# Optimization experiments

Measured on AMD Instinct MI355X. Metric: run time of the kernel, lower is better.

## Reference

```python
import jax, jax.numpy as jnp
import numpy as np
from jax import lax

INV_SQRT2 = np.float32(1.0 / np.sqrt(2.0))

def conv2d(x, w, b=None, stride=1, pad=0):
    y = lax.conv_general_dilated(x, w, (stride, stride), [(pad, pad), (pad, pad)],
                                 dimension_numbers=('NCHW', 'OIHW', 'NCHW'))
    return y if b is None else y + b[None, :, None, None]

def haar_dwt2_zero(x):
    # pytorch_wavelets DWTForward(J=1, wave='haar', mode='zero') for odd H,W:
    # pad one zero at the end of each spatial dim, then pairwise Haar analysis.
    x = jnp.pad(x, ((0, 0), (0, 0), (0, 1), (0, 1)))
    xe, xo = x[..., 0::2], x[..., 1::2]
    lo_w, hi_w = (xe + xo) * INV_SQRT2, (xe - xo) * INV_SQRT2
    def rows(t):
        te, to = t[:, :, 0::2, :], t[:, :, 1::2, :]
        return (te + to) * INV_SQRT2, (te - to) * INV_SQRT2
    ll, lh = rows(lo_w)
    hl, hh = rows(hi_w)
    return ll, lh, hl, hh  # cA, cH, cV, cD

def pixel_shuffle2(x):
    B, C, H, W = x.shape
    co = C // 4
    return x.reshape(B, co, 2, 2, H, W).transpose(0, 1, 4, 2, 5, 3).reshape(B, co, H * 2, W * 2)

def gaussian_kernel5(sigma=0.5):
    r = np.arange(5, dtype=np.float64) - 2.0
    k = np.exp(-(r ** 2) / (2.0 * sigma * sigma))
    return jnp.asarray((k / k.sum()).astype(np.float32))

_GK = gaussian_kernel5(0.5)

def gaussian_blur5(x4d):
    # cv2.GaussianBlur ksize=(5,5) sigma=0.5, default BORDER_REFLECT_101 -> 'reflect' pad
    p = jnp.pad(x4d, ((0, 0), (0, 0), (2, 2), (2, 2)), mode='reflect')
    p = conv2d(p, _GK.reshape(1, 1, 5, 1))
    return conv2d(p, _GK.reshape(1, 1, 1, 5))

def channel_attention(x, w1, w2):
    avg = jnp.mean(x, axis=(2, 3), keepdims=True)
    mx = jnp.max(x, axis=(2, 3), keepdims=True)
    mlp = lambda v: conv2d(jax.nn.relu(conv2d(v, w1)), w2)
    return jax.nn.sigmoid(mlp(avg) + mlp(mx)) * x

def _forward(x, w_x1, b_x1, w_x2, b_x2, w_x3, b_x3, w_hi, b_hi, w_lo, b_lo,
             ca1_w1, ca1_w2, ca2_w1, ca2_w2, w_cat, b_cat, w_c9a, b_c9a, w_c9b, b_c9b):
    f1 = jax.nn.relu(conv2d(x, w_x1, b_x1))            # (1,16,H,W)
    f2 = jax.nn.relu(conv2d(f1, w_x2, b_x2))           # (1,8,H,W)
    tmp12 = jax.nn.relu(conv2d(f2, w_x3, b_x3))        # (1,1,H,W)
    cA, cH, cV, cD = haar_dwt2_zero(tmp12)             # each (1,1,(H+1)/2,(W+1)/2)
    hf = pixel_shuffle2(jax.nn.relu(conv2d(jnp.concatenate([cH, cV, cD], 1), w_hi, b_hi, pad=1)))
    lf = pixel_shuffle2(jax.nn.relu(conv2d(cA, w_lo, b_lo, pad=1)))  # (1,1,H+5,W+5)
    # original detaches hf (cpu->numpy->cv2->cuda): gradients do not flow through it
    hf = gaussian_blur5(lax.stop_gradient(hf))
    hf = channel_attention(hf, ca1_w1, ca1_w2)
    lf = channel_attention(lf, ca2_w1, ca2_w2)
    alpha = 1.0
    cat = jax.nn.relu(conv2d(jnp.concatenate([alpha * hf, (1.0 - alpha) * lf], 1), w_cat, b_cat))
    f12 = tmp12 + cat                                   # (1,1,H,W)
    h = jax.nn.relu(conv2d(f12, w_c9a, b_c9a, pad=1))   # (1,32,H,W)
    return jax.nn.relu(conv2d(h, w_c9b, b_c9b, pad=1))  # (1,64,H,W)

def setup_inputs() -> dict:
    key = jax.random.key(0)
    ks = jax.random.split(key, 24)
    f32 = jnp.float32
    n = lambda k, s, sc=0.05: jax.random.normal(k, s, f32) * sc
    H = W = 511
    return {
        'x': jax.random.normal(ks[0], (1, 204, H, W), f32),
        'w_x1': n(ks[1], (16, 204, 1, 1)), 'b_x1': n(ks[2], (16,)),
        'w_x2': n(ks[3], (8, 16, 1, 1)),   'b_x2': n(ks[4], (8,)),
        'w_x3': n(ks[5], (1, 8, 1, 1)),    'b_x3': n(ks[6], (1,)),
        'w_hi': n(ks[7], (4, 3, 1, 1)),    'b_hi': n(ks[8], (4,)),
        'w_lo': n(ks[9], (4, 1, 1, 1)),    'b_lo': n(ks[10], (4,)),
        'ca1_w1': n(ks[11], (1, 1, 1, 1), 0.5), 'ca1_w2': n(ks[12], (1, 1, 1, 1), 0.5),
        'ca2_w1': n(ks[13], (1, 1, 1, 1), 0.5), 'ca2_w2': n(ks[14], (1, 1, 1, 1), 0.5),
        'w_cat': n(ks[15], (1, 2, 6, 6)),  'b_cat': n(ks[16], (1,)),
        'w_c9a': n(ks[17], (32, 1, 3, 3)), 'b_c9a': n(ks[18], (32,)),
        'w_c9b': n(ks[19], (64, 32, 3, 3)), 'b_c9b': n(ks[20], (64,)),
    }

def reference(x, w_x1, b_x1, w_x2, b_x2, w_x3, b_x3, w_hi, b_hi, w_lo, b_lo,
              ca1_w1, ca1_w2, ca2_w1, ca2_w2, w_cat, b_cat, w_c9a, b_c9a, w_c9b, b_c9b):
    return _forward(x, w_x1, b_x1, w_x2, b_x2, w_x3, b_x3, w_hi, b_hi, w_lo, b_lo,
                    ca1_w1, ca1_w2, ca2_w1, ca2_w2, w_cat, b_cat, w_c9a, b_c9a, w_c9b, b_c9b)
```

## Files before the change

kernel.cpp:

```cpp
#include <hip/hip_runtime.h>
#include <math.h>

#define NP 261121
#define WPX 520

typedef __attribute__((ext_vector_type(8))) short short8;
typedef __attribute__((ext_vector_type(4))) float f32x4;

static __device__ __forceinline__ unsigned short f2bf(float f) {
    unsigned int u = __builtin_bit_cast(unsigned int, f);
    u += 0x7FFFu + ((u >> 16) & 1u);
    return (unsigned short)(u >> 16);
}

__global__ __launch_bounds__(256) void k_prep(const float* __restrict__ w_c9a,
                                              const float* __restrict__ w_c9b,
                                              float* __restrict__ wTa,
                                              unsigned short* __restrict__ wb2)
{
    int t = blockIdx.x * 256 + threadIdx.x;
    if (t < 288) {
        int o = t & 31, k = t >> 5;
        wTa[t] = w_c9a[o * 9 + k];
    }
    if (t < 18432) {
        int o = t / 288, ck = t - o * 288;
        int c = ck / 9, k = ck - c * 9;
        wb2[k * 2048 + o * 32 + c] = f2bf(w_c9b[t]);
    }
}

__global__ __launch_bounds__(256) void k_zero(unsigned short* __restrict__ h2)
{
    int t = blockIdx.x * 256 + threadIdx.x;
    const int ROWN = WPX * 32;
    if (t < 2 * ROWN) {
        int r = t / ROWN;
        h2[(r ? 512 : 0) * ROWN + (t % ROWN)] = 0;
    }
    int u = t - 2 * ROWN;
    if (u >= 0 && u < 511 * 96) {
        int row = u / 96 + 1, cc = u - (u / 96) * 96;
        int col = (cc < 32) ? 0 : (cc < 64 ? 512 : 513);
        h2[(row * WPX + col) * 32 + (cc & 31)] = 0;
    }
}

__global__ __launch_bounds__(256) void k_conv123(const float* __restrict__ x,
                                                 const float* __restrict__ w1,
                                                 const float* __restrict__ b1,
                                                 const float* __restrict__ w2,
                                                 const float* __restrict__ b2,
                                                 const float* __restrict__ w3,
                                                 const float* __restrict__ b3,
                                                 float* __restrict__ tmp12)
{
    __shared__ float s_w1[204 * 16];
    __shared__ float s_misc[192];
    int t = threadIdx.x;
    for (int i = t; i < 204 * 16; i += 256)
        s_w1[i] = w1[(i & 15) * 204 + (i >> 4)];
    if (t < 128) s_misc[t] = w2[t];
    else if (t < 136) s_misc[t] = w3[t - 128];
    else if (t < 152) s_misc[t] = b1[t - 136];
    else if (t < 160) s_misc[t] = b2[t - 152];
    else if (t == 160) s_misc[160] = b3[0];
    __syncthreads();

    int p = blockIdx.x * 256 + t;
    if (p >= NP) return;

    float acc[16];
#pragma unroll
    for (int o = 0; o < 16; ++o) acc[o] = 0.f;

    const float* xp = x + p;
#pragma unroll 4
    for (int c = 0; c < 204; ++c) {
        float xv = xp[(size_t)c * NP];
        const float4* wv = reinterpret_cast<const float4*>(s_w1 + c * 16);
        float wl[16];
        *reinterpret_cast<float4*>(&wl[0])  = wv[0];
        *reinterpret_cast<float4*>(&wl[4])  = wv[1];
        *reinterpret_cast<float4*>(&wl[8])  = wv[2];
        *reinterpret_cast<float4*>(&wl[12]) = wv[3];
#pragma unroll
        for (int o = 0; o < 16; ++o) acc[o] = fmaf(xv, wl[o], acc[o]);
    }

    float f1[16];
#pragma unroll
    for (int o = 0; o < 16; ++o) f1[o] = fmaxf(acc[o] + s_misc[136 + o], 0.f);

    float tmp = s_misc[160];
#pragma unroll
    for (int j = 0; j < 8; ++j) {
        float s = s_misc[152 + j];
#pragma unroll
        for (int o = 0; o < 16; ++o) s = fmaf(f1[o], s_misc[j * 16 + o], s);
        tmp = fmaf(fmaxf(s, 0.f), s_misc[128 + j], tmp);
    }
    tmp12[p] = fmaxf(tmp, 0.f);
}

__global__ __launch_bounds__(256) void k_dwt_hi(const float* __restrict__ tmp12,
                                                const float* __restrict__ w_hi,
                                                const float* __restrict__ b_hi,
                                                float* __restrict__ hf)
{
    const float INV = 0.70710678118654752440f;
    int idx = blockIdx.x * 256 + threadIdx.x;
    if (idx >= 258 * 258) return;
    int h = idx / 258, w = idx - h * 258;

    float wh[12], bh[4];
#pragma unroll
    for (int i = 0; i < 12; ++i) wh[i] = w_hi[i];
#pragma unroll
    for (int o = 0; o < 4; ++o) bh[o] = b_hi[o];

    float v[4];
    if (h == 0 || h == 257 || w == 0 || w == 257) {
#pragma unroll
        for (int o = 0; o < 4; ++o) v[o] = fmaxf(bh[o], 0.f);
    } else {
        int hh = h - 1, ww = w - 1;
        int r0 = 2 * hh, r1 = 2 * hh + 1, c0 = 2 * ww, c1 = 2 * ww + 1;
        float a = tmp12[r0 * 511 + c0];
        float b = (c1 < 511) ? tmp12[r0 * 511 + c1] : 0.f;
        float c = (r1 < 511) ? tmp12[r1 * 511 + c0] : 0.f;
        float d = (r1 < 511 && c1 < 511) ? tmp12[r1 * 511 + c1] : 0.f;
        float lo0 = (a + b) * INV, hi0 = (a - b) * INV;
        float lo1 = (c + d) * INV, hi1 = (c - d) * INV;
        float cH = (lo0 - lo1) * INV;
        float cV = (hi0 + hi1) * INV;
        float cD = (hi0 - hi1) * INV;
#pragma unroll
        for (int o = 0; o < 4; ++o)
            v[o] = fmaxf(wh[o * 3 + 0] * cH + wh[o * 3 + 1] * cV + wh[o * 3 + 2] * cD + bh[o], 0.f);
    }
    int orow = (2 * h) * 516 + 2 * w;
    hf[orow]       = v[0];
    hf[orow + 1]   = v[1];
    hf[orow + 516] = v[2];
    hf[orow + 517] = v[3];
}

__global__ __launch_bounds__(256) void k_blur(const float* __restrict__ hf,
                                              float* __restrict__ hfb,
                                              float g0, float g1, float g2)
{
    int idx = blockIdx.x * 256 + threadIdx.x;
    if (idx >= 516 * 516) return;
    int y = idx / 516, x = idx - y * 516;
    float g[5] = {g0, g1, g2, g1, g0};
    int ry[5], rx[5];
#pragma unroll
    for (int i = 0; i < 5; ++i) {
        int yy = y + i - 2; yy = yy < 0 ? -yy : (yy > 515 ? 1030 - yy : yy);
        int xx = x + i - 2; xx = xx < 0 ? -xx : (xx > 515 ? 1030 - xx : xx);
        ry[i] = yy * 516; rx[i] = xx;
    }
    float s = 0.f;
#pragma unroll
    for (int i = 0; i < 5; ++i) {
        float rs = 0.f;
#pragma unroll
        for (int j = 0; j < 5; ++j) rs = fmaf(g[j], hf[ry[i] + rx[j]], rs);
        s = fmaf(g[i], rs, s);
    }
    hfb[idx] = s;
}

__global__ __launch_bounds__(256) void k_red1(const float* __restrict__ hfb,
                                              float* __restrict__ psum,
                                              float* __restrict__ pmax)
{
    __shared__ float ss[256], sm[256];
    int t = threadIdx.x;
    int gid = blockIdx.x * 256 + t;
    float s = 0.f, m = -3.4e38f;
    for (int i = gid; i < 516 * 516; i += 65536) { float v = hfb[i]; s += v; m = fmaxf(m, v); }
    ss[t] = s; sm[t] = m;
    __syncthreads();
    for (int off = 128; off > 0; off >>= 1) {
        if (t < off) { ss[t] += ss[t + off]; sm[t] = fmaxf(sm[t], sm[t + off]); }
        __syncthreads();
    }
    if (t == 0) { psum[blockIdx.x] = ss[0]; pmax[blockIdx.x] = sm[0]; }
}

__global__ __launch_bounds__(256) void k_red2(const float* __restrict__ psum,
                                              const float* __restrict__ pmax,
                                              const float* __restrict__ caw1,
                                              const float* __restrict__ caw2,
                                              float* __restrict__ scale)
{
    __shared__ float ss[256], sm[256];
    int t = threadIdx.x;
    ss[t] = psum[t]; sm[t] = pmax[t];
    __syncthreads();
    for (int off = 128; off > 0; off >>= 1) {
        if (t < off) { ss[t] += ss[t + off]; sm[t] = fmaxf(sm[t], sm[t + off]); }
        __syncthreads();
    }
    if (t == 0) {
        float avg = ss[0] / 266256.f;
        float mx = sm[0];
        float a = caw1[0], b = caw2[0];
        float z = b * fmaxf(a * avg, 0.f) + b * fmaxf(a * mx, 0.f);
        scale[0] = 1.f / (1.f + expf(-z));
    }
}

__global__ __launch_bounds__(256) void k_cat(const float* __restrict__ hfb,
                                             const float* __restrict__ tmp12,
                                             const float* __restrict__ w_cat,
                                             const float* __restrict__ b_cat,
                                             const float* __restrict__ scale,
                                             float* __restrict__ f12)
{
    int p = blockIdx.x * 256 + threadIdx.x;
    if (p >= NP) return;
    int y = p / 511, x = p - y * 511;
    float sc = scale[0];
    float s = 0.f;
#pragma unroll
    for (int ky = 0; ky < 6; ++ky) {
        const float* row = hfb + (y + ky) * 516 + x;
#pragma unroll
        for (int kx = 0; kx < 6; ++kx) s = fmaf(row[kx], w_cat[ky * 6 + kx], s);
    }
    f12[p] = tmp12[p] + fmaxf(sc * s + b_cat[0], 0.f);
}

__global__ __launch_bounds__(256) void k_c9a(const float* __restrict__ f12,
                                             const float* __restrict__ wTa,
                                             const float* __restrict__ bias,
                                             unsigned short* __restrict__ h2)
{
    int p = blockIdx.x * 256 + threadIdx.x;
    if (p >= NP) return;
    int y = p / 511, x = p - y * 511;
    float hv[9];
#pragma unroll
    for (int ky = 0; ky < 3; ++ky)
#pragma unroll
        for (int kx = 0; kx < 3; ++kx) {
            int yy = y + ky - 1, xx = x + kx - 1;
            hv[ky * 3 + kx] = (yy >= 0 && yy < 511 && xx >= 0 && xx < 511) ? f12[yy * 511 + xx] : 0.f;
        }
    float acc[32];
#pragma unroll
    for (int o = 0; o < 32; ++o) acc[o] = bias[o];
#pragma unroll
    for (int k = 0; k < 9; ++k) {
        float v = hv[k];
        const float* wp = wTa + k * 32;
#pragma unroll
        for (int o = 0; o < 32; ++o) acc[o] = fmaf(v, wp[o], acc[o]);
    }
    unsigned short o16[32];
#pragma unroll
    for (int o = 0; o < 32; ++o) o16[o] = f2bf(fmaxf(acc[o], 0.f));
    unsigned short* dst = h2 + ((size_t)(y + 1) * WPX + (x + 1)) * 32;
#pragma unroll
    for (int i = 0; i < 4; ++i)
        reinterpret_cast<short8*>(dst)[i] = reinterpret_cast<const short8*>(o16)[i];
}

__global__ __launch_bounds__(256, 2) void k_c9b(const unsigned short* __restrict__ h2,
                                                const unsigned short* __restrict__ wb2,
                                                const float* __restrict__ bias,
                                                float* __restrict__ out)
{
    int wave = threadIdx.x >> 6, lane = threadIdx.x & 63;
    int y  = blockIdx.x >> 1;
    int xh = blockIdx.x & 1;
    int xb = xh * 256 + wave * 64;
    int lpx = lane & 15, kg = lane >> 4;

    f32x4 acc[4][4];
#pragma unroll
    for (int m = 0; m < 4; ++m)
#pragma unroll
        for (int n = 0; n < 4; ++n) acc[m][n] = (f32x4){0.f, 0.f, 0.f, 0.f};

    const int base = (((y + 1) * WPX) + (xb + 1) + lpx) * 32 + kg * 8;

#pragma unroll
    for (int kt = 0; kt < 9; ++kt) {
        const int dy = kt / 3 - 1, dx = kt % 3 - 1;
        const int toff = (dy * WPX + dx) * 32;

        short8 a[4], b[4];
        const short8* wp = reinterpret_cast<const short8*>(wb2 + kt * 2048 + kg * 8);
#pragma unroll
        for (int m = 0; m < 4; ++m) a[m] = wp[(m * 16 + lpx) * 4];
#pragma unroll
        for (int n = 0; n < 4; ++n)
            b[n] = *reinterpret_cast<const short8*>(h2 + base + toff + n * 512);
#pragma unroll
        for (int m = 0; m < 4; ++m)
#pragma unroll
            for (int n = 0; n < 4; ++n)
                acc[m][n] = __builtin_amdgcn_mfma_f32_16x16x32_bf16(a[m], b[n], acc[m][n], 0, 0, 0);
    }

    const int ybase = y * 511;
#pragma unroll
    for (int m = 0; m < 4; ++m) {
#pragma unroll
        for (int r = 0; r < 4; ++r) {
            int o = m * 16 + kg * 4 + r;
            float bo = bias[o];
#pragma unroll
            for (int n = 0; n < 4; ++n) {
                int px = xb + n * 16 + lpx;
                if (px < 511)
                    out[(size_t)o * NP + ybase + px] = fmaxf(acc[m][n][r] + bo, 0.f);
            }
        }
    }
}

extern "C" void kernel_launch(void* const* d_in, const int* in_sizes, int n_in,
                              void* d_out, int out_size, void* d_ws, size_t ws_size,
                              hipStream_t stream)
{
    (void)in_sizes; (void)n_in; (void)out_size; (void)ws_size;

    const float* x     = (const float*)d_in[0];
    const float* w_x1  = (const float*)d_in[1];
    const float* b_x1  = (const float*)d_in[2];
    const float* w_x2  = (const float*)d_in[3];
    const float* b_x2  = (const float*)d_in[4];
    const float* w_x3  = (const float*)d_in[5];
    const float* b_x3  = (const float*)d_in[6];
    const float* w_hi  = (const float*)d_in[7];
    const float* b_hi  = (const float*)d_in[8];
    const float* ca1w1 = (const float*)d_in[11];
    const float* ca1w2 = (const float*)d_in[12];
    const float* w_cat = (const float*)d_in[15];
    const float* b_cat = (const float*)d_in[16];
    const float* w_c9a = (const float*)d_in[17];
    const float* b_c9a = (const float*)d_in[18];
    const float* w_c9b = (const float*)d_in[19];
    const float* b_c9b = (const float*)d_in[20];

    float* ws    = (float*)d_ws;
    float* tmp12 = ws + 0;
    float* hf    = ws + 261184;
    float* hfb   = ws + 527488;
    float* f12   = ws + 793792;
    float* psum  = ws + 1054976;
    float* pmax  = ws + 1055232;
    float* scale = ws + 1055488;
    float* wTa   = ws + 1055552;
    unsigned short* wb2 = (unsigned short*)(ws + 1055872);
    unsigned short* h2  = (unsigned short*)(ws + 1065088);

    float* out = (float*)d_out;

    double kk[5], ssum = 0.0;
    for (int i = 0; i < 5; ++i) { double r = i - 2.0; kk[i] = exp(-r * r / 0.5); ssum += kk[i]; }
    float g0 = (float)(kk[0] / ssum), g1 = (float)(kk[1] / ssum), g2 = (float)(kk[2] / ssum);

    k_prep<<<72, 256, 0, stream>>>(w_c9a, w_c9b, wTa, wb2);
    k_zero<<<322, 256, 0, stream>>>(h2);
    k_conv123<<<1021, 256, 0, stream>>>(x, w_x1, b_x1, w_x2, b_x2, w_x3, b_x3, tmp12);
    k_dwt_hi<<<261, 256, 0, stream>>>(tmp12, w_hi, b_hi, hf);
    k_blur<<<1041, 256, 0, stream>>>(hf, hfb, g0, g1, g2);
    k_red1<<<256, 256, 0, stream>>>(hfb, psum, pmax);
    k_red2<<<1, 256, 0, stream>>>(psum, pmax, ca1w1, ca1w2, scale);
    k_cat<<<1021, 256, 0, stream>>>(hfb, tmp12, w_cat, b_cat, scale, f12);
    k_c9a<<<1021, 256, 0, stream>>>(f12, wTa, b_c9a, h2);
    k_c9b<<<1022, 256, 0, stream>>>(h2, wb2, b_c9b, out);
}
```

Before: 123.4 us.

## Split h2 into channel planes, remap c9b blocks per XCD, merge zero kernel

The intermediate h2 buffer moves from pixel-interleaved 32 channels to four planes of 8 channels each, so each MFMA B-operand load in k_c9b reads a contiguous 16-byte chunk within a plane. Block IDs in k_c9b are remapped so consecutive rows land on the same XCD, which is meant to improve L2 reuse of the overlapping stencil rows. The halo-zeroing kernel is folded into k_prep, saving a launch. k_conv123 drops its LDS staging and instead reads a pretransposed weight array from global memory, relying on the scalar cache. This risks register pressure and slower weight reads in conv123.

```diff
diff --git a/kernel.cpp b/kernel.cpp
--- a/kernel.cpp
+++ b/kernel.cpp
@@ -1,8 +1,10 @@
 #include <hip/hip_runtime.h>
 #include <math.h>
 
-#define NP 261121
-#define WPX 520
+#define NP   261121
+#define WPX  520
+#define ROWN 4160
+#define PSTR 2138240
 
 typedef __attribute__((ext_vector_type(8))) short short8;
 typedef __attribute__((ext_vector_type(4))) float f32x4;
@@ -15,39 +17,40 @@
 
 __global__ __launch_bounds__(256) void k_prep(const float* __restrict__ w_c9a,
                                               const float* __restrict__ w_c9b,
+                                              const float* __restrict__ w_x1,
                                               float* __restrict__ wTa,
-                                              unsigned short* __restrict__ wb2)
+                                              unsigned short* __restrict__ wb2,
+                                              float* __restrict__ wT1,
+                                              unsigned short* __restrict__ h2)
 {
     int t = blockIdx.x * 256 + threadIdx.x;
-    if (t < 288) {
-        int o = t & 31, k = t >> 5;
-        wTa[t] = w_c9a[o * 9 + k];
-    }
+    if (t < 288)  wTa[t] = w_c9a[(t & 31) * 9 + (t >> 5)];
+    if (t < 3264) wT1[t] = w_x1[(t & 15) * 204 + (t >> 4)];
     if (t < 18432) {
         int o = t / 288, ck = t - o * 288;
         int c = ck / 9, k = ck - c * 9;
         wb2[k * 2048 + o * 32 + c] = f2bf(w_c9b[t]);
     }
-}
-
-__global__ __launch_bounds__(256) void k_zero(unsigned short* __restrict__ h2)
-{
-    int t = blockIdx.x * 256 + threadIdx.x;
-    const int ROWN = WPX * 32;
-    if (t < 2 * ROWN) {
-        int r = t / ROWN;
-        h2[(r ? 512 : 0) * ROWN + (t % ROWN)] = 0;
-    }
-    int u = t - 2 * ROWN;
-    if (u >= 0 && u < 511 * 96) {
-        int row = u / 96 + 1, cc = u - (u / 96) * 96;
-        int col = (cc < 32) ? 0 : (cc < 64 ? 512 : 513);
-        h2[(row * WPX + col) * 32 + (cc & 31)] = 0;
+    short8 z8 = {0, 0, 0, 0, 0, 0, 0, 0};
+    if (t < 4160) {
+        int pl = t / 1040;
+        int rr = t - pl * 1040;
+        int row = rr >= 520 ? 512 : 0;
+        int ch  = rr >= 520 ? rr - 520 : rr;
+        *reinterpret_cast<short8*>(h2 + (size_t)pl * PSTR + (size_t)row * ROWN + ch * 8) = z8;
+    }
+    int z = t - 4160;
+    if (z >= 0 && z < 6132) {
+        int row = z / 12 + 1;
+        int j = z - (row - 1) * 12;
+        int pl = j / 3, cidx = j - pl * 3;
+        int col = (cidx == 0) ? 0 : (cidx == 1 ? 512 : 513);
+        *reinterpret_cast<short8*>(h2 + (size_t)pl * PSTR + (size_t)row * ROWN + col * 8) = z8;
     }
 }
 
 __global__ __launch_bounds__(256) void k_conv123(const float* __restrict__ x,
-                                                 const float* __restrict__ w1,
+                                                 const float* __restrict__ wT1,
                                                  const float* __restrict__ b1,
                                                  const float* __restrict__ w2,
                                                  const float* __restrict__ b2,
@@ -55,52 +58,35 @@
                                                  const float* __restrict__ b3,
                                                  float* __restrict__ tmp12)
 {
-    __shared__ float s_w1[204 * 16];
-    __shared__ float s_misc[192];
-    int t = threadIdx.x;
-    for (int i = t; i < 204 * 16; i += 256)
-        s_w1[i] = w1[(i & 15) * 204 + (i >> 4)];
-    if (t < 128) s_misc[t] = w2[t];
-    else if (t < 136) s_misc[t] = w3[t - 128];
-    else if (t < 152) s_misc[t] = b1[t - 136];
-    else if (t < 160) s_misc[t] = b2[t - 152];
-    else if (t == 160) s_misc[160] = b3[0];
-    __syncthreads();
-
-    int p = blockIdx.x * 256 + t;
-    if (p >= NP) return;
+    int p0 = blockIdx.x * 256 + threadIdx.x;
+    int p = p0 < NP ? p0 : NP - 1;
 
     float acc[16];
 #pragma unroll
     for (int o = 0; o < 16; ++o) acc[o] = 0.f;
 
     const float* xp = x + p;
-#pragma unroll 4
+#pragma unroll 2
     for (int c = 0; c < 204; ++c) {
-        float xv = xp[(size_t)c * NP];
-        const float4* wv = reinterpret_cast<const float4*>(s_w1 + c * 16);
-        float wl[16];
-        *reinterpret_cast<float4*>(&wl[0])  = wv[0];
-        *reinterpret_cast<float4*>(&wl[4])  = wv[1];
-        *reinterpret_cast<float4*>(&wl[8])  = wv[2];
-        *reinterpret_cast<float4*>(&wl[12]) = wv[3];
-#pragma unroll
-        for (int o = 0; o < 16; ++o) acc[o] = fmaf(xv, wl[o], acc[o]);
+        float xv = xp[c * NP];
+        const float* wp = wT1 + c * 16;
+#pragma unroll
+        for (int o = 0; o < 16; ++o) acc[o] = fmaf(xv, wp[o], acc[o]);
     }
 
     float f1[16];
 #pragma unroll
-    for (int o = 0; o < 16; ++o) f1[o] = fmaxf(acc[o] + s_misc[136 + o], 0.f);
-
-    float tmp = s_misc[160];
+    for (int o = 0; o < 16; ++o) f1[o] = fmaxf(acc[o] + b1[o], 0.f);
+
+    float tmp = b3[0];
 #pragma unroll
     for (int j = 0; j < 8; ++j) {
-        float s = s_misc[152 + j];
-#pragma unroll
-        for (int o = 0; o < 16; ++o) s = fmaf(f1[o], s_misc[j * 16 + o], s);
-        tmp = fmaf(fmaxf(s, 0.f), s_misc[128 + j], tmp);
-    }
-    tmp12[p] = fmaxf(tmp, 0.f);
+        float s = b2[j];
+#pragma unroll
+        for (int o = 0; o < 16; ++o) s = fmaf(f1[o], w2[j * 16 + o], s);
+        tmp = fmaf(fmaxf(s, 0.f), w3[j], tmp);
+    }
+    if (p0 < NP) tmp12[p0] = fmaxf(tmp, 0.f);
 }
 
 __global__ __launch_bounds__(256) void k_dwt_hi(const float* __restrict__ tmp12,
@@ -263,10 +249,11 @@
     unsigned short o16[32];
 #pragma unroll
     for (int o = 0; o < 32; ++o) o16[o] = f2bf(fmaxf(acc[o], 0.f));
-    unsigned short* dst = h2 + ((size_t)(y + 1) * WPX + (x + 1)) * 32;
+    size_t px = (size_t)(y + 1) * WPX + (x + 1);
 #pragma unroll
     for (int i = 0; i < 4; ++i)
-        reinterpret_cast<short8*>(dst)[i] = reinterpret_cast<const short8*>(o16)[i];
+        *reinterpret_cast<short8*>(h2 + (size_t)i * PSTR + px * 8) =
+            reinterpret_cast<const short8*>(o16)[i];
 }
 
 __global__ __launch_bounds__(256, 2) void k_c9b(const unsigned short* __restrict__ h2,
@@ -274,9 +261,14 @@
                                                 const float* __restrict__ bias,
                                                 float* __restrict__ out)
 {
+    int bid = blockIdx.x;
+    int xcd = bid & 7, jj = bid >> 3;
+    const int q = 127, r = 6;
+    int wg = (xcd < r ? xcd * (q + 1) : r * (q + 1) + (xcd - r) * q) + jj;
+
     int wave = threadIdx.x >> 6, lane = threadIdx.x & 63;
-    int y  = blockIdx.x >> 1;
-    int xh = blockIdx.x & 1;
+    int y  = wg >> 1;
+    int xh = wg & 1;
     int xb = xh * 256 + wave * 64;
     int lpx = lane & 15, kg = lane >> 4;
 
@@ -286,12 +278,13 @@
 #pragma unroll
         for (int n = 0; n < 4; ++n) acc[m][n] = (f32x4){0.f, 0.f, 0.f, 0.f};
 
-    const int base = (((y + 1) * WPX) + (xb + 1) + lpx) * 32 + kg * 8;
+    const size_t pbase = (size_t)kg * PSTR;
+    const int base_px = (y + 1) * WPX + (xb + 1) + lpx;
 
 #pragma unroll
     for (int kt = 0; kt < 9; ++kt) {
         const int dy = kt / 3 - 1, dx = kt % 3 - 1;
-        const int toff = (dy * WPX + dx) * 32;
+        const int tpx = dy * WPX + dx;
 
         short8 a[4], b[4];
         const short8* wp = reinterpret_cast<const short8*>(wb2 + kt * 2048 + kg * 8);
@@ -299,7 +292,7 @@
         for (int m = 0; m < 4; ++m) a[m] = wp[(m * 16 + lpx) * 4];
 #pragma unroll
         for (int n = 0; n < 4; ++n)
-            b[n] = *reinterpret_cast<const short8*>(h2 + base + toff + n * 512);
+            b[n] = *reinterpret_cast<const short8*>(h2 + pbase + (size_t)(base_px + tpx + n * 16) * 8);
 #pragma unroll
         for (int m = 0; m < 4; ++m)
 #pragma unroll
@@ -311,14 +304,14 @@
 #pragma unroll
     for (int m = 0; m < 4; ++m) {
 #pragma unroll
-        for (int r = 0; r < 4; ++r) {
-            int o = m * 16 + kg * 4 + r;
+        for (int rr = 0; rr < 4; ++rr) {
+            int o = m * 16 + kg * 4 + rr;
             float bo = bias[o];
 #pragma unroll
             for (int n = 0; n < 4; ++n) {
                 int px = xb + n * 16 + lpx;
                 if (px < 511)
-                    out[(size_t)o * NP + ybase + px] = fmaxf(acc[m][n][r] + bo, 0.f);
+                    out[(size_t)o * NP + ybase + px] = fmaxf(acc[m][n][rr] + bo, 0.f);
             }
         }
     }
@@ -357,8 +350,9 @@
     float* pmax  = ws + 1055232;
     float* scale = ws + 1055488;
     float* wTa   = ws + 1055552;
-    unsigned short* wb2 = (unsigned short*)(ws + 1055872);
-    unsigned short* h2  = (unsigned short*)(ws + 1065088);
+    float* wT1   = ws + 1055872;
+    unsigned short* wb2 = (unsigned short*)(ws + 1059200);
+    unsigned short* h2  = (unsigned short*)(ws + 1068416);
 
     float* out = (float*)d_out;
 
@@ -366,9 +360,8 @@
     for (int i = 0; i < 5; ++i) { double r = i - 2.0; kk[i] = exp(-r * r / 0.5); ssum += kk[i]; }
     float g0 = (float)(kk[0] / ssum), g1 = (float)(kk[1] / ssum), g2 = (float)(kk[2] / ssum);
 
-    k_prep<<<72, 256, 0, stream>>>(w_c9a, w_c9b, wTa, wb2);
-    k_zero<<<322, 256, 0, stream>>>(h2);
-    k_conv123<<<1021, 256, 0, stream>>>(x, w_x1, b_x1, w_x2, b_x2, w_x3, b_x3, tmp12);
+    k_prep<<<72, 256, 0, stream>>>(w_c9a, w_c9b, w_x1, wTa, wb2, wT1, h2);
+    k_conv123<<<1021, 256, 0, stream>>>(x, wT1, b_x1, w_x2, b_x2, w_x3, b_x3, tmp12);
     k_dwt_hi<<<261, 256, 0, stream>>>(tmp12, w_hi, b_hi, hf);
     k_blur<<<1041, 256, 0, stream>>>(hf, hfb, g0, g1, g2);
     k_red1<<<256, 256, 0, stream>>>(hfb, psum, pmax);
```

Measured after the change: 139.5 us. 13.1% more time.
